# Optimization experiments

Hardware: AMD Instinct MI355X
Metric: run time of the kernel (lower is better)

Reference implementation:

```python
import jax, jax.numpy as jnp
import numpy as np

N_NODES = 50000
N_EDGES = 1600000
D_IN = 64
D_HID = 64
N_CLASSES = 10
N_GRAPHS = 64


def setup_inputs() -> dict:
    key = jax.random.key(0)
    ks = jax.random.split(key, 9)
    x = jax.random.normal(ks[0], (N_NODES, D_IN), dtype=jnp.float32)
    edge_index = jax.random.randint(ks[1], (2, N_EDGES), 0, N_NODES, dtype=jnp.int64)
    batch = jnp.sort(jax.random.randint(ks[2], (N_NODES,), 0, N_GRAPHS, dtype=jnp.int64))
    s1 = 1.0 / np.sqrt(D_IN)
    s2 = 1.0 / np.sqrt(D_HID)
    W1 = jax.random.uniform(ks[3], (D_IN, D_HID), jnp.float32, -s1, s1)
    b1 = jnp.zeros((D_HID,), jnp.float32)
    W2 = jax.random.uniform(ks[4], (D_HID, D_HID), jnp.float32, -s2, s2)
    b2 = jnp.zeros((D_HID,), jnp.float32)
    Wfc = jax.random.uniform(ks[5], (D_HID, N_CLASSES), jnp.float32, -s2, s2)
    bfc = jnp.zeros((N_CLASSES,), jnp.float32)
    return {"x": x, "edge_index": edge_index, "batch": batch,
            "W1": W1, "b1": b1, "W2": W2, "b2": b2, "Wfc": Wfc, "bfc": bfc}


def _gcn_conv(h, src, dst, deg_inv_sqrt, W, b):
    # h: [N, d_in] -> linear then normalized scatter-add aggregation (PyG GCNConv)
    h = h @ W                                   # [N, d_out]
    norm = deg_inv_sqrt[src] * deg_inv_sqrt[dst]  # [E+N]
    msg = h[src] * norm[:, None]                # gather + scale  [E+N, d_out]
    out = jax.ops.segment_sum(msg, dst, num_segments=h.shape[0])
    return out + b


def reference(x, edge_index, batch, W1, b1, W2, b2, Wfc, bfc):
    n = x.shape[0]
    loops = jnp.arange(n, dtype=edge_index.dtype)
    src = jnp.concatenate([edge_index[0], loops])  # self-loops appended
    dst = jnp.concatenate([edge_index[1], loops])
    deg = jax.ops.segment_sum(jnp.ones_like(dst, x.dtype), dst, num_segments=n)
    deg_inv_sqrt = jnp.where(deg > 0, jax.lax.rsqrt(deg), 0.0)

    h = jax.nn.relu(_gcn_conv(x, src, dst, deg_inv_sqrt, W1, b1))
    # dropout is identity in eval mode
    h = jax.nn.relu(_gcn_conv(h, src, dst, deg_inv_sqrt, W2, b2))

    # global mean pool over graphs
    sums = jax.ops.segment_sum(h, batch, num_segments=N_GRAPHS)      # [G, d]
    cnts = jax.ops.segment_sum(jnp.ones((n,), h.dtype), batch, num_segments=N_GRAPHS)
    pooled = sums / jnp.maximum(cnts, 1.0)[:, None]
    return pooled @ Wfc + bfc                                        # [G, classes]
```

## Files before the change

kernel.cpp:

```cpp
#include <hip/hip_runtime.h>
#include <hip/hip_bf16.h>

#define THREADS 256
#define PART_T 8192
#define NF_PAD 1024

__global__ void detect_i64(const unsigned* __restrict__ raw, int* __restrict__ flag) {
    __shared__ int nz;
    if (threadIdx.x == 0) nz = 0;
    __syncthreads();
    int found = 0;
    for (int i = threadIdx.x; i < 2048; i += blockDim.x) {
        if (raw[2 * i + 1] != 0u) found = 1;
    }
    if (found) atomicOr(&nz, 1);
    __syncthreads();
    if (threadIdx.x == 0) *flag = nz ? 0 : 1;
}

__global__ void convert_idx(const int* __restrict__ raw, int* __restrict__ out,
                            int n, const int* __restrict__ flag) {
    int i = blockIdx.x * blockDim.x + threadIdx.x;
    if (i < n) out[i] = (*flag) ? raw[2 * i] : raw[i];
}

__global__ __launch_bounds__(256) void bucket_hist(const int* __restrict__ raw, int E,
                                                   int NF, int* __restrict__ bh,
                                                   const int* __restrict__ flag) {
    __shared__ int h[NF_PAD];
    int t = threadIdx.x;
    for (int i = t; i < NF_PAD; i += 256) h[i] = 0;
    __syncthreads();
    bool f64 = (*flag) != 0;
    long long base = (long long)blockIdx.x * PART_T;
    long long lim = base + PART_T;
    if (lim > (long long)E) lim = E;
    for (long long e = base + t; e < lim; e += 256) {
        int d = f64 ? raw[2 * ((long long)E + e)] : raw[E + e];
        atomicAdd(&h[d >> 6], 1);
    }
    __syncthreads();
    for (int i = t; i < NF; i += 256) {
        int v = h[i];
        if (v) atomicAdd(&bh[i], v);
    }
}

__global__ __launch_bounds__(1024) void bucket_scan(const int* __restrict__ bh,
                                                    int NF, int E, int n,
                                                    int* __restrict__ boff,
                                                    int* __restrict__ gcur,
                                                    int* __restrict__ noff) {
    __shared__ int h[NF_PAD];
    int t = threadIdx.x;
    h[t] = (t < NF) ? bh[t] : 0;
    __syncthreads();
    int v = h[t];
    for (int o = 1; o < 1024; o <<= 1) {
        int x = (t >= o) ? h[t - o] : 0;
        __syncthreads();
        h[t] += x;
        __syncthreads();
    }
    int exc = h[t] - v;
    if (t <= NF) boff[t] = (t == NF) ? E : exc;
    if (t < NF) gcur[t] = exc;
    if (t == 0) noff[n] = E;
}

__global__ __launch_bounds__(256) void partition_edges(const int* __restrict__ raw, int E,
                                                       int NF, int* __restrict__ gcur,
                                                       unsigned* __restrict__ elist,
                                                       const int* __restrict__ flag) {
    __shared__ int cnt[NF_PAD];
    __shared__ int pfx[NF_PAD];
    __shared__ int gbase[NF_PAD];
    __shared__ int tsum[256];
    __shared__ unsigned stage[PART_T];
    int t = threadIdx.x;
    long long base = (long long)blockIdx.x * PART_T;
    int tileN = (int)min((long long)PART_T, (long long)E - base);
    bool f64 = (*flag) != 0;

    for (int i = t; i < NF_PAD; i += 256) cnt[i] = 0;
    __syncthreads();

    unsigned pk[PART_T / 256];
#pragma unroll
    for (int k = 0; k < PART_T / 256; k++) {
        long long e = base + k * 256 + t;
        if (e < (long long)E) {
            int s = f64 ? raw[2 * e] : raw[e];
            int d = f64 ? raw[2 * ((long long)E + e)] : raw[E + e];
            unsigned p = (unsigned)s | ((unsigned)d << 16);
            pk[k] = p;
            atomicAdd(&cnt[d >> 6], 1);
        } else {
            pk[k] = 0xFFFFFFFFu;
        }
    }
    __syncthreads();

    int a0 = cnt[4 * t], a1 = cnt[4 * t + 1], a2 = cnt[4 * t + 2], a3 = cnt[4 * t + 3];
    int tot = a0 + a1 + a2 + a3;
    tsum[t] = tot;
    __syncthreads();
    for (int o = 1; o < 256; o <<= 1) {
        int x = (t >= o) ? tsum[t - o] : 0;
        __syncthreads();
        tsum[t] += x;
        __syncthreads();
    }
    int pre = tsum[t] - tot;
    pfx[4 * t] = pre;
    pfx[4 * t + 1] = pre + a0;
    pfx[4 * t + 2] = pre + a0 + a1;
    pfx[4 * t + 3] = pre + a0 + a1 + a2;

    for (int i = t; i < NF; i += 256) {
        gbase[i] = (cnt[i] > 0) ? atomicAdd(&gcur[i], cnt[i]) : 0;
    }
    __syncthreads();
    for (int i = t; i < NF_PAD; i += 256) cnt[i] = 0;
    __syncthreads();

#pragma unroll
    for (int k = 0; k < PART_T / 256; k++) {
        long long e = base + k * 256 + t;
        if (e < (long long)E) {
            unsigned p = pk[k];
            int f = p >> 22;
            int r = atomicAdd(&cnt[f], 1);
            stage[pfx[f] + r] = p;
        }
    }
    __syncthreads();

    for (int i = t; i < tileN; i += 256) {
        unsigned v = stage[i];
        int f = v >> 22;
        elist[gbase[f] + (i - pfx[f])] = v;
    }
}

__global__ __launch_bounds__(256) void bucket_csr(const unsigned* __restrict__ elist,
                                                  const int* __restrict__ boff,
                                                  int n,
                                                  unsigned short* __restrict__ ssrc,
                                                  int* __restrict__ noff,
                                                  float* __restrict__ dis) {
    __shared__ int cnt[64];
    __shared__ int cur[64];
    int b = blockIdx.x;
    int t = threadIdx.x;
    int beg = boff[b], end = boff[b + 1];
    if (t < 64) cnt[t] = 0;
    __syncthreads();
    for (int e = beg + t; e < end; e += 256) {
        unsigned v = elist[e];
        atomicAdd(&cnt[(v >> 16) & 63], 1);
    }
    __syncthreads();
    if (t < 64) {
        int d = cnt[t];
        int v = d;
#pragma unroll
        for (int o = 1; o < 64; o <<= 1) {
            int x = __shfl_up(v, o, 64);
            if (t >= o) v += x;
        }
        int exc = beg + v - d;
        cur[t] = exc;
        int node = b * 64 + t;
        if (node <= n) noff[node] = exc;
        if (node < n) dis[node] = rsqrtf((float)(d + 1));
    }
    __syncthreads();
    for (int e = beg + t; e < end; e += 256) {
        unsigned v = elist[e];
        int pos = atomicAdd(&cur[(v >> 16) & 63], 1);
        ssrc[pos] = (unsigned short)(v & 0xFFFFu);
    }
}

__global__ __launch_bounds__(256) void linear64(const float* __restrict__ in,
                                                const float* __restrict__ W,
                                                const float* __restrict__ dis,
                                                __hip_bfloat16* __restrict__ outH, int n) {
    __shared__ float sIn[4][64];
    int t = threadIdx.x;
    int ln = t >> 6, od = t & 63;
    float w[64];
#pragma unroll
    for (int k = 0; k < 64; k++) w[k] = W[k * 64 + od];
    int base = blockIdx.x * 64;
    for (int pass = 0; pass < 16; pass++) {
        int node0 = base + pass * 4;
        __syncthreads();
        {
            int nd = node0 + ln;
            sIn[ln][od] = (nd < n) ? in[(long long)nd * 64 + od] : 0.f;
        }
        __syncthreads();
        int node = node0 + ln;
        if (node < n) {
            float acc = 0.f;
#pragma unroll
            for (int k = 0; k < 64; k++) acc += sIn[ln][k] * w[k];
            outH[(long long)node * 64 + od] = __float2bfloat16(acc * dis[node]);
        }
    }
}

__device__ __forceinline__ float bf_lo(unsigned u) { return __uint_as_float(u << 16); }
__device__ __forceinline__ float bf_hi(unsigned u) { return __uint_as_float(u & 0xFFFF0000u); }

__global__ __launch_bounds__(256) void gather_agg(const unsigned short* __restrict__ hs,
                                                  const int* __restrict__ noff,
                                                  const unsigned short* __restrict__ ssrc,
                                                  const float* __restrict__ dis,
                                                  const float* __restrict__ bias,
                                                  float* __restrict__ out, int n) {
    int t = threadIdx.x;
    int lane = t & 63;
    int g = lane >> 3;
    int l = lane & 7;
    int node = blockIdx.x * 4 + (t >> 6);
    if (node >= n) return;
    int beg = noff[node], end = noff[node + 1];
    float a0 = 0.f, a1 = 0.f, a2 = 0.f, a3 = 0.f, a4 = 0.f, a5 = 0.f, a6 = 0.f, a7 = 0.f;

    for (int c = beg; c < end; c += 64) {
        int cnt = min(64, end - c);
        int myidx = (lane < cnt) ? (int)ssrc[c + lane] : 0;
#pragma unroll 2
        for (int j = 0; j < cnt; j += 8) {
            int s = __shfl(myidx, j + g, 64);
            uint4 v = ((const uint4*)(hs + (long long)s * 64))[l];
            if (j + g < cnt) {
                a0 += bf_lo(v.x); a1 += bf_hi(v.x);
                a2 += bf_lo(v.y); a3 += bf_hi(v.y);
                a4 += bf_lo(v.z); a5 += bf_hi(v.z);
                a6 += bf_lo(v.w); a7 += bf_hi(v.w);
            }
        }
    }
    if (g == 0) {
        uint4 v = ((const uint4*)(hs + (long long)node * 64))[l];
        a0 += bf_lo(v.x); a1 += bf_hi(v.x);
        a2 += bf_lo(v.y); a3 += bf_hi(v.y);
        a4 += bf_lo(v.z); a5 += bf_hi(v.z);
        a6 += bf_lo(v.w); a7 += bf_hi(v.w);
    }
#pragma unroll
    for (int o = 8; o <= 32; o <<= 1) {
        a0 += __shfl_xor(a0, o, 64);
        a1 += __shfl_xor(a1, o, 64);
        a2 += __shfl_xor(a2, o, 64);
        a3 += __shfl_xor(a3, o, 64);
        a4 += __shfl_xor(a4, o, 64);
        a5 += __shfl_xor(a5, o, 64);
        a6 += __shfl_xor(a6, o, 64);
        a7 += __shfl_xor(a7, o, 64);
    }
    if (g == 0) {
        float dv = dis[node];
        const float4* bp = (const float4*)bias;
        float4 b0 = bp[2 * l], b1 = bp[2 * l + 1];
        float4 r0, r1;
        r0.x = dv * a0 + b0.x; r0.x = r0.x > 0.f ? r0.x : 0.f;
        r0.y = dv * a1 + b0.y; r0.y = r0.y > 0.f ? r0.y : 0.f;
        r0.z = dv * a2 + b0.z; r0.z = r0.z > 0.f ? r0.z : 0.f;
        r0.w = dv * a3 + b0.w; r0.w = r0.w > 0.f ? r0.w : 0.f;
        r1.x = dv * a4 + b1.x; r1.x = r1.x > 0.f ? r1.x : 0.f;
        r1.y = dv * a5 + b1.y; r1.y = r1.y > 0.f ? r1.y : 0.f;
        r1.z = dv * a6 + b1.z; r1.z = r1.z > 0.f ? r1.z : 0.f;
        r1.w = dv * a7 + b1.w; r1.w = r1.w > 0.f ? r1.w : 0.f;
        float4* op = (float4*)(out + (long long)node * 64);
        op[2 * l] = r0;
        op[2 * l + 1] = r1;
    }
}

__global__ __launch_bounds__(256) void pool_sum(const float* __restrict__ h,
                                                const int* __restrict__ batch,
                                                float* __restrict__ psum,
                                                int* __restrict__ pcnt, int n) {
    int t = threadIdx.x;
    int lane = t & 63;
    int base = (blockIdx.x * 4 + (t >> 6)) * 32;
    float acc = 0.f;
    int g = -1, cnt = 0;
    for (int i = 0; i < 32; i++) {
        int node = base + i;
        if (node >= n) break;
        int bg = batch[node];
        if (bg != g) {
            if (g >= 0) {
                atomicAdd(&psum[g * 64 + lane], acc);
                if (lane == 0) atomicAdd(&pcnt[g], cnt);
            }
            g = bg; acc = 0.f; cnt = 0;
        }
        acc += h[(long long)node * 64 + lane];
        cnt++;
    }
    if (g >= 0) {
        atomicAdd(&psum[g * 64 + lane], acc);
        if (lane == 0) atomicAdd(&pcnt[g], cnt);
    }
}

__global__ __launch_bounds__(640) void final_fc(const float* __restrict__ psum,
                                                const int* __restrict__ pcnt,
                                                const float* __restrict__ Wfc,
                                                const float* __restrict__ bfc,
                                                float* __restrict__ out) {
    __shared__ float sP[64 * 64];
    __shared__ float sW[64 * 10];
    int t = threadIdx.x;
    for (int i = t; i < 4096; i += 640) sP[i] = psum[i];
    if (t < 640) sW[t] = Wfc[t];
    __syncthreads();
    int g = t / 10, c = t % 10;
    float acc = 0.f;
#pragma unroll
    for (int k = 0; k < 64; k++) acc += sP[g * 64 + k] * sW[k * 10 + c];
    float cnt = (float)pcnt[g];
    if (cnt < 1.f) cnt = 1.f;
    out[g * 10 + c] = acc / cnt + bfc[c];
}

static inline int cdiv(long long a, int b) { return (int)((a + b - 1) / b); }

extern "C" void kernel_launch(void* const* d_in, const int* in_sizes, int n_in,
                              void* d_out, int out_size, void* d_ws, size_t ws_size,
                              hipStream_t stream) {
    const float* x    = (const float*)d_in[0];
    const int*   eraw = (const int*)d_in[1];
    const int*   braw = (const int*)d_in[2];
    const float* W1   = (const float*)d_in[3];
    const float* b1   = (const float*)d_in[4];
    const float* W2   = (const float*)d_in[5];
    const float* b2   = (const float*)d_in[6];
    const float* Wfc  = (const float*)d_in[7];
    const float* bfc  = (const float*)d_in[8];
    float* out = (float*)d_out;

    const int N  = in_sizes[0] / 64;
    const int E  = in_sizes[1] / 2;
    const int NF = cdiv(N, 64);

    char* p = (char*)d_ws;
    auto carve = [&](size_t bytes) { char* q = p; p += (bytes + 255) / 256 * 256; return q; };
    int*            flag   = (int*)carve(4);
    unsigned*       elist  = (unsigned*)carve((size_t)E * sizeof(unsigned));
    unsigned short* ssrc   = (unsigned short*)carve((size_t)E * sizeof(unsigned short));
    int*            batchi = (int*)carve((size_t)N * sizeof(int));
    int*            bh     = (int*)carve((size_t)NF * sizeof(int));
    int*            boff   = (int*)carve((size_t)(NF + 1) * sizeof(int));
    int*            gcur   = (int*)carve((size_t)NF * sizeof(int));
    int*            noff   = (int*)carve((size_t)(NF * 64 + 1) * sizeof(int));
    float*          dis    = (float*)carve((size_t)N * sizeof(float));
    __hip_bfloat16* bufH   = (__hip_bfloat16*)carve((size_t)N * 64 * sizeof(__hip_bfloat16));
    float*          bufA   = (float*)carve((size_t)N * 64 * sizeof(float));
    float*          bufB   = (float*)carve((size_t)N * 64 * sizeof(float));
    float*          psum   = (float*)carve(64 * 64 * sizeof(float));
    int*            pcnt   = (int*)carve(64 * sizeof(int));

    hipMemsetAsync(bh, 0, (size_t)NF * sizeof(int), stream);
    hipMemsetAsync(psum, 0, 64 * 64 * sizeof(float), stream);
    hipMemsetAsync(pcnt, 0, 64 * sizeof(int), stream);

    detect_i64<<<1, THREADS, 0, stream>>>((const unsigned*)eraw, flag);
    convert_idx<<<cdiv(N, THREADS), THREADS, 0, stream>>>(braw, batchi, N, flag);

    bucket_hist<<<cdiv(E, PART_T), 256, 0, stream>>>(eraw, E, NF, bh, flag);
    bucket_scan<<<1, 1024, 0, stream>>>(bh, NF, E, N, boff, gcur, noff);
    partition_edges<<<cdiv(E, PART_T), 256, 0, stream>>>(eraw, E, NF, gcur, elist, flag);
    bucket_csr<<<NF, 256, 0, stream>>>(elist, boff, N, ssrc, noff, dis);

    linear64<<<cdiv(N, 64), 256, 0, stream>>>(x, W1, dis, bufH, N);
    gather_agg<<<cdiv(N, 4), 256, 0, stream>>>((const unsigned short*)bufH, noff, ssrc, dis, b1, bufA, N);

    linear64<<<cdiv(N, 64), 256, 0, stream>>>(bufA, W2, dis, bufH, N);
    gather_agg<<<cdiv(N, 4), 256, 0, stream>>>((const unsigned short*)bufH, noff, ssrc, dis, b2, bufB, N);

    pool_sum<<<cdiv(N, 128), 256, 0, stream>>>(bufB, batchi, psum, pcnt, N);
    final_fc<<<1, 640, 0, stream>>>(psum, pcnt, Wfc, bfc, out);
}
```

Baseline: 271.9 us.

## Split hidden features into two half-width gathers and fuse prep kernels

Stores the bf16 hidden features as two separate 32-column arrays, and runs the neighbour gather twice, once per half. Each half is 3.2 MB instead of 6.4 MB, so it is more likely to stay in cache during the random gathers. The int64-format detection moves into each kernel and is merged with batch conversion and buffer zeroing, which removes three memsets and two launches. The partition tile size is also halved. The cost is that the edge lists are read twice per layer, gather launches double, and every block of the bucket kernels repeats the detection reads.

```diff
diff --git a/kernel.cpp b/kernel.cpp
--- a/kernel.cpp
+++ b/kernel.cpp
@@ -2,38 +2,52 @@
 #include <hip/hip_bf16.h>
 
 #define THREADS 256
-#define PART_T 8192
+#define HIST_T 8192
+#define PART_T 4096
 #define NF_PAD 1024
 
-__global__ void detect_i64(const unsigned* __restrict__ raw, int* __restrict__ flag) {
+__device__ __forceinline__ bool detect_f64_block(const unsigned* __restrict__ raw,
+                                                 int E2, int* nz, int t) {
+    if (t == 0) *nz = 0;
+    __syncthreads();
+    int found = 0;
+    int lim = E2 < 2048 ? E2 : 2048;
+#pragma unroll
+    for (int k = 0; k < 8; k++) {
+        int i = t * 8 + k;
+        if (i < lim) found |= (raw[2 * i + 1] != 0u);
+    }
+    if (found) atomicOr(nz, 1);
+    __syncthreads();
+    return (*nz) == 0;
+}
+
+__global__ __launch_bounds__(256) void prep(const int* __restrict__ eraw, int E,
+                                            const int* __restrict__ braw,
+                                            int* __restrict__ batchi, int n,
+                                            int* __restrict__ bh, int NF,
+                                            float* __restrict__ psum,
+                                            int* __restrict__ pcnt) {
     __shared__ int nz;
-    if (threadIdx.x == 0) nz = 0;
-    __syncthreads();
-    int found = 0;
-    for (int i = threadIdx.x; i < 2048; i += blockDim.x) {
-        if (raw[2 * i + 1] != 0u) found = 1;
-    }
-    if (found) atomicOr(&nz, 1);
-    __syncthreads();
-    if (threadIdx.x == 0) *flag = nz ? 0 : 1;
-}
-
-__global__ void convert_idx(const int* __restrict__ raw, int* __restrict__ out,
-                            int n, const int* __restrict__ flag) {
-    int i = blockIdx.x * blockDim.x + threadIdx.x;
-    if (i < n) out[i] = (*flag) ? raw[2 * i] : raw[i];
+    int t = threadIdx.x;
+    bool f64 = detect_f64_block((const unsigned*)eraw, 2 * E, &nz, t);
+    int gid = blockIdx.x * 256 + t;
+    if (gid < n) batchi[gid] = f64 ? braw[2 * gid] : braw[gid];
+    if (gid < NF) bh[gid] = 0;
+    if (gid < 4096) psum[gid] = 0.f;
+    if (gid < 64) pcnt[gid] = 0;
 }
 
 __global__ __launch_bounds__(256) void bucket_hist(const int* __restrict__ raw, int E,
-                                                   int NF, int* __restrict__ bh,
-                                                   const int* __restrict__ flag) {
+                                                   int NF, int* __restrict__ bh) {
     __shared__ int h[NF_PAD];
-    int t = threadIdx.x;
+    __shared__ int nz;
+    int t = threadIdx.x;
+    bool f64 = detect_f64_block((const unsigned*)raw, 2 * E, &nz, t);
     for (int i = t; i < NF_PAD; i += 256) h[i] = 0;
     __syncthreads();
-    bool f64 = (*flag) != 0;
-    long long base = (long long)blockIdx.x * PART_T;
-    long long lim = base + PART_T;
+    long long base = (long long)blockIdx.x * HIST_T;
+    long long lim = base + HIST_T;
     if (lim > (long long)E) lim = E;
     for (long long e = base + t; e < lim; e += 256) {
         int d = f64 ? raw[2 * ((long long)E + e)] : raw[E + e];
@@ -70,17 +84,17 @@
 
 __global__ __launch_bounds__(256) void partition_edges(const int* __restrict__ raw, int E,
                                                        int NF, int* __restrict__ gcur,
-                                                       unsigned* __restrict__ elist,
-                                                       const int* __restrict__ flag) {
+                                                       unsigned* __restrict__ elist) {
     __shared__ int cnt[NF_PAD];
     __shared__ int pfx[NF_PAD];
     __shared__ int gbase[NF_PAD];
     __shared__ int tsum[256];
     __shared__ unsigned stage[PART_T];
-    int t = threadIdx.x;
+    __shared__ int nz;
+    int t = threadIdx.x;
+    bool f64 = detect_f64_block((const unsigned*)raw, 2 * E, &nz, t);
     long long base = (long long)blockIdx.x * PART_T;
     int tileN = (int)min((long long)PART_T, (long long)E - base);
-    bool f64 = (*flag) != 0;
 
     for (int i = t; i < NF_PAD; i += 256) cnt[i] = 0;
     __syncthreads();
@@ -186,7 +200,8 @@
 __global__ __launch_bounds__(256) void linear64(const float* __restrict__ in,
                                                 const float* __restrict__ W,
                                                 const float* __restrict__ dis,
-                                                __hip_bfloat16* __restrict__ outH, int n) {
+                                                __hip_bfloat16* __restrict__ hA,
+                                                __hip_bfloat16* __restrict__ hB, int n) {
     __shared__ float sIn[4][64];
     int t = threadIdx.x;
     int ln = t >> 6, od = t & 63;
@@ -207,7 +222,9 @@
             float acc = 0.f;
 #pragma unroll
             for (int k = 0; k < 64; k++) acc += sIn[ln][k] * w[k];
-            outH[(long long)node * 64 + od] = __float2bfloat16(acc * dis[node]);
+            __hip_bfloat16 hv = __float2bfloat16(acc * dis[node]);
+            if (od < 32) hA[(long long)node * 32 + od] = hv;
+            else         hB[(long long)node * 32 + (od - 32)] = hv;
         }
     }
 }
@@ -215,16 +232,16 @@
 __device__ __forceinline__ float bf_lo(unsigned u) { return __uint_as_float(u << 16); }
 __device__ __forceinline__ float bf_hi(unsigned u) { return __uint_as_float(u & 0xFFFF0000u); }
 
-__global__ __launch_bounds__(256) void gather_agg(const unsigned short* __restrict__ hs,
-                                                  const int* __restrict__ noff,
-                                                  const unsigned short* __restrict__ ssrc,
-                                                  const float* __restrict__ dis,
-                                                  const float* __restrict__ bias,
-                                                  float* __restrict__ out, int n) {
+__global__ __launch_bounds__(256) void gather_half(const unsigned short* __restrict__ hs,
+                                                   const int* __restrict__ noff,
+                                                   const unsigned short* __restrict__ ssrc,
+                                                   const float* __restrict__ dis,
+                                                   const float* __restrict__ bias,
+                                                   float* __restrict__ out, int n, int half) {
     int t = threadIdx.x;
     int lane = t & 63;
-    int g = lane >> 3;
-    int l = lane & 7;
+    int g = lane >> 2;
+    int l = lane & 3;
     int node = blockIdx.x * 4 + (t >> 6);
     if (node >= n) return;
     int beg = noff[node], end = noff[node + 1];
@@ -233,10 +250,9 @@
     for (int c = beg; c < end; c += 64) {
         int cnt = min(64, end - c);
         int myidx = (lane < cnt) ? (int)ssrc[c + lane] : 0;
-#pragma unroll 2
-        for (int j = 0; j < cnt; j += 8) {
+        for (int j = 0; j < cnt; j += 16) {
             int s = __shfl(myidx, j + g, 64);
-            uint4 v = ((const uint4*)(hs + (long long)s * 64))[l];
+            uint4 v = ((const uint4*)(hs + (long long)s * 32))[l];
             if (j + g < cnt) {
                 a0 += bf_lo(v.x); a1 += bf_hi(v.x);
                 a2 += bf_lo(v.y); a3 += bf_hi(v.y);
@@ -246,14 +262,14 @@
         }
     }
     if (g == 0) {
-        uint4 v = ((const uint4*)(hs + (long long)node * 64))[l];
+        uint4 v = ((const uint4*)(hs + (long long)node * 32))[l];
         a0 += bf_lo(v.x); a1 += bf_hi(v.x);
         a2 += bf_lo(v.y); a3 += bf_hi(v.y);
         a4 += bf_lo(v.z); a5 += bf_hi(v.z);
         a6 += bf_lo(v.w); a7 += bf_hi(v.w);
     }
 #pragma unroll
-    for (int o = 8; o <= 32; o <<= 1) {
+    for (int o = 4; o <= 32; o <<= 1) {
         a0 += __shfl_xor(a0, o, 64);
         a1 += __shfl_xor(a1, o, 64);
         a2 += __shfl_xor(a2, o, 64);
@@ -266,7 +282,7 @@
     if (g == 0) {
         float dv = dis[node];
         const float4* bp = (const float4*)bias;
-        float4 b0 = bp[2 * l], b1 = bp[2 * l + 1];
+        float4 b0 = bp[half * 8 + 2 * l], b1 = bp[half * 8 + 2 * l + 1];
         float4 r0, r1;
         r0.x = dv * a0 + b0.x; r0.x = r0.x > 0.f ? r0.x : 0.f;
         r0.y = dv * a1 + b0.y; r0.y = r0.y > 0.f ? r0.y : 0.f;
@@ -276,9 +292,9 @@
         r1.y = dv * a5 + b1.y; r1.y = r1.y > 0.f ? r1.y : 0.f;
         r1.z = dv * a6 + b1.z; r1.z = r1.z > 0.f ? r1.z : 0.f;
         r1.w = dv * a7 + b1.w; r1.w = r1.w > 0.f ? r1.w : 0.f;
-        float4* op = (float4*)(out + (long long)node * 64);
-        op[2 * l] = r0;
-        op[2 * l + 1] = r1;
+        float4* op = (float4*)(out + (long long)node * 64 + half * 32 + l * 8);
+        op[0] = r0;
+        op[1] = r1;
     }
 }
 
@@ -353,7 +369,6 @@
 
     char* p = (char*)d_ws;
     auto carve = [&](size_t bytes) { char* q = p; p += (bytes + 255) / 256 * 256; return q; };
-    int*            flag   = (int*)carve(4);
     unsigned*       elist  = (unsigned*)carve((size_t)E * sizeof(unsigned));
     unsigned short* ssrc   = (unsigned short*)carve((size_t)E * sizeof(unsigned short));
     int*            batchi = (int*)carve((size_t)N * sizeof(int));
@@ -362,29 +377,27 @@
     int*            gcur   = (int*)carve((size_t)NF * sizeof(int));
     int*            noff   = (int*)carve((size_t)(NF * 64 + 1) * sizeof(int));
     float*          dis    = (float*)carve((size_t)N * sizeof(float));
-    __hip_bfloat16* bufH   = (__hip_bfloat16*)carve((size_t)N * 64 * sizeof(__hip_bfloat16));
+    __hip_bfloat16* hA     = (__hip_bfloat16*)carve((size_t)N * 32 * sizeof(__hip_bfloat16));
+    __hip_bfloat16* hB     = (__hip_bfloat16*)carve((size_t)N * 32 * sizeof(__hip_bfloat16));
     float*          bufA   = (float*)carve((size_t)N * 64 * sizeof(float));
     float*          bufB   = (float*)carve((size_t)N * 64 * sizeof(float));
     float*          psum   = (float*)carve(64 * 64 * sizeof(float));
     int*            pcnt   = (int*)carve(64 * sizeof(int));
 
-    hipMemsetAsync(bh, 0, (size_t)NF * sizeof(int), stream);
-    hipMemsetAsync(psum, 0, 64 * 64 * sizeof(float), stream);
-    hipMemsetAsync(pcnt, 0, 64 * sizeof(int), stream);
-
-    detect_i64<<<1, THREADS, 0, stream>>>((const unsigned*)eraw, flag);
-    convert_idx<<<cdiv(N, THREADS), THREADS, 0, stream>>>(braw, batchi, N, flag);
-
-    bucket_hist<<<cdiv(E, PART_T), 256, 0, stream>>>(eraw, E, NF, bh, flag);
+    prep<<<cdiv(N, 256), 256, 0, stream>>>(eraw, E, braw, batchi, N, bh, NF, psum, pcnt);
+
+    bucket_hist<<<cdiv(E, HIST_T), 256, 0, stream>>>(eraw, E, NF, bh);
     bucket_scan<<<1, 1024, 0, stream>>>(bh, NF, E, N, boff, gcur, noff);
-    partition_edges<<<cdiv(E, PART_T), 256, 0, stream>>>(eraw, E, NF, gcur, elist, flag);
+    partition_edges<<<cdiv(E, PART_T), 256, 0, stream>>>(eraw, E, NF, gcur, elist);
     bucket_csr<<<NF, 256, 0, stream>>>(elist, boff, N, ssrc, noff, dis);
 
-    linear64<<<cdiv(N, 64), 256, 0, stream>>>(x, W1, dis, bufH, N);
-    gather_agg<<<cdiv(N, 4), 256, 0, stream>>>((const unsigned short*)bufH, noff, ssrc, dis, b1, bufA, N);
-
-    linear64<<<cdiv(N, 64), 256, 0, stream>>>(bufA, W2, dis, bufH, N);
-    gather_agg<<<cdiv(N, 4), 256, 0, stream>>>((const unsigned short*)bufH, noff, ssrc, dis, b2, bufB, N);
+    linear64<<<cdiv(N, 64), 256, 0, stream>>>(x, W1, dis, hA, hB, N);
+    gather_half<<<cdiv(N, 4), 256, 0, stream>>>((const unsigned short*)hA, noff, ssrc, dis, b1, bufA, N, 0);
+    gather_half<<<cdiv(N, 4), 256, 0, stream>>>((const unsigned short*)hB, noff, ssrc, dis, b1, bufA, N, 1);
+
+    linear64<<<cdiv(N, 64), 256, 0, stream>>>(bufA, W2, dis, hA, hB, N);
+    gather_half<<<cdiv(N, 4), 256, 0, stream>>>((const unsigned short*)hA, noff, ssrc, dis, b2, bufB, N, 0);
+    gather_half<<<cdiv(N, 4), 256, 0, stream>>>((const unsigned short*)hB, noff, ssrc, dis, b2, bufB, N, 1);
 
     pool_sum<<<cdiv(N, 128), 256, 0, stream>>>(bufB, batchi, psum, pcnt, N);
     final_fc<<<1, 640, 0, stream>>>(psum, pcnt, Wfc, bfc, out);
```

Result: slower. 301.8 us (+11.0%).
